# Performance work log

Measured on AMD Instinct MI355X. Metric: run time of the kernel, lower is better.

## Reference

```python
import jax, jax.numpy as jnp
import numpy as np

D = 1024
H = 16
F = 4096
EPS = 1e-6


def _layernorm(x, alpha, bias):
    # Faithful to torch: unbiased std (ddof=1), divide by (std + eps)
    mean = jnp.mean(x, axis=-1, keepdims=True)
    std = jnp.std(x, axis=-1, keepdims=True, ddof=1)
    return alpha * (x - mean) / (std + EPS) + bias


def setup_inputs() -> dict:
    key = jax.random.key(0)
    ks = jax.random.split(key, 12)
    B, S = 2, 2048
    s = 1.0 / np.sqrt(D)
    inp = {
        "x": jax.random.normal(ks[0], (B, S, D), jnp.float32),
        "mask": jnp.ones((B, 1, 1, S), jnp.int32),
        "wq": jax.random.normal(ks[1], (D, D), jnp.float32) * s,
        "bq": jnp.zeros((D,), jnp.float32),
        "wk": jax.random.normal(ks[2], (D, D), jnp.float32) * s,
        "bk": jnp.zeros((D,), jnp.float32),
        "wv": jax.random.normal(ks[3], (D, D), jnp.float32) * s,
        "bv": jnp.zeros((D,), jnp.float32),
        "wo": jax.random.normal(ks[4], (D, D), jnp.float32) * s,
        "bo": jnp.zeros((D,), jnp.float32),
        "ln1_a": jnp.ones((D,), jnp.float32),
        "ln1_b": jnp.zeros((D,), jnp.float32),
        "ln2_a": jnp.ones((D,), jnp.float32),
        "ln2_b": jnp.zeros((D,), jnp.float32),
        "w1": jax.random.normal(ks[5], (D, F), jnp.float32) * s,
        "b1": jnp.zeros((F,), jnp.float32),
        "w2": jax.random.normal(ks[6], (F, D), jnp.float32) * (1.0 / np.sqrt(F)),
        "b2": jnp.zeros((D,), jnp.float32),
    }
    return inp


def reference(x, mask, wq, bq, wk, bk, wv, bv, wo, bo,
              ln1_a, ln1_b, ln2_a, ln2_b, w1, b1, w2, b2):
    B, S, _ = x.shape
    dk = D // H
    # --- residual 1: pre-LN self-attention ---
    h = _layernorm(x, ln1_a, ln1_b)
    q = (h @ wq + bq).reshape(B, S, H, dk).transpose(0, 2, 1, 3)
    k = (h @ wk + bk).reshape(B, S, H, dk).transpose(0, 2, 1, 3)
    v = (h @ wv + bv).reshape(B, S, H, dk).transpose(0, 2, 1, 3)
    scores = jnp.einsum('bhqd,bhkd->bhqk', q, k) / jnp.sqrt(jnp.float32(dk))
    scores = jnp.where(mask == 0, jnp.float32(-1e9), scores)
    attn = jax.nn.softmax(scores, axis=-1)
    ctx = jnp.einsum('bhqk,bhkd->bhqd', attn, v)
    ctx = ctx.transpose(0, 2, 1, 3).reshape(B, S, D)
    x = x + (ctx @ wo + bo)
    # --- residual 2: pre-LN feed-forward ---
    h = _layernorm(x, ln2_a, ln2_b)
    ff = jax.nn.relu(h @ w1 + b1) @ w2 + b2
    return x + ff
```

## Files before the change

### kernel.cpp

```cpp
#include <hip/hip_runtime.h>
#include <hip/hip_bf16.h>
#include <math.h>

typedef __attribute__((ext_vector_type(8))) short bf16x8;
typedef __attribute__((ext_vector_type(4))) float f32x4;
typedef unsigned int uint32;
typedef __attribute__((ext_vector_type(2))) unsigned int uint32x2;

#define DMODEL 1024
#define SEQ    2048
#define NB     2
#define NH     16
#define HD     64
#define FDIM   4096
#define NTOK   (NB*SEQ)

__device__ __forceinline__ void async16(const void* g, void* s) {
    __builtin_amdgcn_global_load_lds((const __attribute__((address_space(1))) unsigned int*)g,
                                     (__attribute__((address_space(3))) unsigned int*)s,
                                     16, 0, 0);
}

__global__ __launch_bounds__(256) void transpose_cvt_k(const float* __restrict__ src,
                                                       __hip_bfloat16* __restrict__ dst,
                                                       int R, int C) {
    __shared__ __hip_bfloat16 tile[32][33];
    int tx = threadIdx.x, ty = threadIdx.y;
    int bx = blockIdx.x * 32, by = blockIdx.y * 32;
    for (int i = 0; i < 32; i += 8)
        tile[ty + i][tx] = __float2bfloat16(src[(size_t)(by + ty + i) * C + bx + tx]);
    __syncthreads();
    for (int i = 0; i < 32; i += 8)
        dst[(size_t)(bx + ty + i) * R + by + tx] = tile[tx][ty + i];
}

__global__ __launch_bounds__(256) void ln_kernel(const float* __restrict__ x,
                                                 const float* __restrict__ alpha,
                                                 const float* __restrict__ beta,
                                                 __hip_bfloat16* __restrict__ out) {
    const int row = blockIdx.x, tid = threadIdx.x;
    const size_t base = (size_t)row * DMODEL;
    float v[4];
    for (int e = 0; e < 4; ++e) v[e] = x[base + tid * 4 + e];
    float s1 = v[0] + v[1] + v[2] + v[3];
    float s2 = v[0]*v[0] + v[1]*v[1] + v[2]*v[2] + v[3]*v[3];
    for (int off = 32; off > 0; off >>= 1) {
        s1 += __shfl_down(s1, off);
        s2 += __shfl_down(s2, off);
    }
    __shared__ float red[8];
    int w = tid >> 6, lane = tid & 63;
    if (lane == 0) { red[w * 2] = s1; red[w * 2 + 1] = s2; }
    __syncthreads();
    if (tid == 0) {
        float a = 0.f, b = 0.f;
        for (int i = 0; i < 4; ++i) { a += red[2 * i]; b += red[2 * i + 1]; }
        red[0] = a; red[1] = b;
    }
    __syncthreads();
    s1 = red[0]; s2 = red[1];
    float mean = s1 * (1.0f / DMODEL);
    float var  = fmaxf((s2 - (float)DMODEL * mean * mean) * (1.0f / (DMODEL - 1)), 0.f);
    float inv  = 1.0f / (sqrtf(var) + 1e-6f);
    for (int e = 0; e < 4; ++e) {
        int c = tid * 4 + e;
        float y = alpha[c] * (v[e] - mean) * inv + beta[c];
        out[base + c] = __float2bfloat16(y);
    }
}

template <int EPI>
__global__ __launch_bounds__(256) void gemm_bt(const __hip_bfloat16* __restrict__ A,
                                               const __hip_bfloat16* __restrict__ Bt,
                                               const float* __restrict__ bias,
                                               const float* __restrict__ res,
                                               void* __restrict__ Cout,
                                               int M, int N, int K) {
    __shared__ alignas(16) __hip_bfloat16 As[2][128 * 32];
    __shared__ alignas(16) __hip_bfloat16 Bs[2][128 * 32];
    const int tid = threadIdx.x, l = tid & 63;
    const int w = tid >> 6;
    const int wm = w >> 1, wn = w & 1, quad = l >> 4, lc = l & 15;
    const int row0 = blockIdx.y * 128, col0 = blockIdx.x * 128;
    const int lr = l >> 2, cb = l & 3;
    const int srow = 32 * w + lr;
    const int scol = (cb ^ ((lr >> 1) & 3)) * 8;
    const int rsw  = (lc >> 1) & 3;

    f32x4 acc[4][4];
    for (int i = 0; i < 4; ++i)
        for (int j = 0; j < 4; ++j) acc[i][j] = (f32x4){0.f, 0.f, 0.f, 0.f};

    for (int c = 0; c < 2; ++c) {
        async16(A  + (size_t)(row0 + srow + 16 * c) * K + scol, (char*)&As[0][0] + w * 2048 + c * 1024);
        async16(Bt + (size_t)(col0 + srow + 16 * c) * K + scol, (char*)&Bs[0][0] + w * 2048 + c * 1024);
    }
    const int NKT = K / 32;
    for (int kt = 0; kt < NKT; ++kt) {
        const int cur = kt & 1;
        __syncthreads();
        if (kt + 1 < NKT) {
            const int k1 = (kt + 1) * 32;
            for (int c = 0; c < 2; ++c) {
                async16(A  + (size_t)(row0 + srow + 16 * c) * K + k1 + scol, (char*)&As[cur ^ 1][0] + w * 2048 + c * 1024);
                async16(Bt + (size_t)(col0 + srow + 16 * c) * K + k1 + scol, (char*)&Bs[cur ^ 1][0] + w * 2048 + c * 1024);
            }
        }
        bf16x8 af[4], bfr[4];
        for (int i = 0; i < 4; ++i) af[i]  = *(const bf16x8*)&As[cur][(64 * wm + 16 * i + lc) * 32 + (quad ^ rsw) * 8];
        for (int j = 0; j < 4; ++j) bfr[j] = *(const bf16x8*)&Bs[cur][(64 * wn + 16 * j + lc) * 32 + (quad ^ rsw) * 8];
        for (int i = 0; i < 4; ++i)
            for (int j = 0; j < 4; ++j)
                acc[i][j] = __builtin_amdgcn_mfma_f32_16x16x32_bf16(af[i], bfr[j], acc[i][j], 0, 0, 0);
    }

    __hip_bfloat16* Cb = (__hip_bfloat16*)Cout;
    float* Cf = (float*)Cout;
    for (int j = 0; j < 4; ++j) {
        int col = col0 + 64 * wn + 16 * j + lc;
        float bv = bias[col];
        for (int i = 0; i < 4; ++i) {
            int rbase = row0 + 64 * wm + 16 * i + quad * 4;
            for (int r = 0; r < 4; ++r) {
                size_t idx = (size_t)(rbase + r) * N + col;
                float vacc = acc[i][j][r] + bv;
                if (EPI == 0)      Cb[idx] = __float2bfloat16(vacc);
                else if (EPI == 1) Cb[idx] = __float2bfloat16(fmaxf(vacc, 0.f));
                else               Cf[idx] = vacc + res[idx];
            }
        }
    }
}

template <int EPI>
__global__ __launch_bounds__(512) void gemm_bt_sk(const __hip_bfloat16* __restrict__ A,
                                                  const __hip_bfloat16* __restrict__ Bt,
                                                  const float* __restrict__ bias,
                                                  const float* __restrict__ res,
                                                  void* __restrict__ Cout,
                                                  int M, int N, int K) {
    __shared__ alignas(16) char smem[65536];
    const int tid = threadIdx.x, l = tid & 63;
    const int w = tid >> 6;
    const int g = w >> 2;
    const int wl = w & 3;
    const int wm = wl >> 1, wn = wl & 1, quad = l >> 4, lc = l & 15;
    const int row0 = blockIdx.y * 128, col0 = blockIdx.x * 128;
    const int lr = l >> 2, cb = l & 3;
    const int srow = 32 * wl + lr;
    const int scol = (cb ^ ((lr >> 1) & 3)) * 8;
    const int rsw  = (lc >> 1) & 3;
    const int Kh = K >> 1;
    const int kbase = g * Kh;

    char* AsBase = smem + (size_t)g * 16384;
    char* BsBase = smem + 32768 + (size_t)g * 16384;

    f32x4 acc[4][4];
    for (int i = 0; i < 4; ++i)
        for (int j = 0; j < 4; ++j) acc[i][j] = (f32x4){0.f, 0.f, 0.f, 0.f};

    for (int c = 0; c < 2; ++c) {
        async16(A  + (size_t)(row0 + srow + 16 * c) * K + kbase + scol, AsBase + wl * 2048 + c * 1024);
        async16(Bt + (size_t)(col0 + srow + 16 * c) * K + kbase + scol, BsBase + wl * 2048 + c * 1024);
    }
    const int NKT = Kh / 32;
    for (int kt = 0; kt < NKT; ++kt) {
        const int cur = kt & 1;
        __syncthreads();
        if (kt + 1 < NKT) {
            const int k1 = kbase + (kt + 1) * 32;
            for (int c = 0; c < 2; ++c) {
                async16(A  + (size_t)(row0 + srow + 16 * c) * K + k1 + scol, AsBase + (cur ^ 1) * 8192 + wl * 2048 + c * 1024);
                async16(Bt + (size_t)(col0 + srow + 16 * c) * K + k1 + scol, BsBase + (cur ^ 1) * 8192 + wl * 2048 + c * 1024);
            }
        }
        const __hip_bfloat16* Asc = (const __hip_bfloat16*)(AsBase + cur * 8192);
        const __hip_bfloat16* Bsc = (const __hip_bfloat16*)(BsBase + cur * 8192);
        bf16x8 af[4], bfr[4];
        for (int i = 0; i < 4; ++i) af[i]  = *(const bf16x8*)&Asc[(64 * wm + 16 * i + lc) * 32 + (quad ^ rsw) * 8];
        for (int j = 0; j < 4; ++j) bfr[j] = *(const bf16x8*)&Bsc[(64 * wn + 16 * j + lc) * 32 + (quad ^ rsw) * 8];
        for (int i = 0; i < 4; ++i)
            for (int j = 0; j < 4; ++j)
                acc[i][j] = __builtin_amdgcn_mfma_f32_16x16x32_bf16(af[i], bfr[j], acc[i][j], 0, 0, 0);
    }

    __syncthreads();
    float* comb = (float*)smem;
    if (g == 1) {
        for (int j = 0; j < 4; ++j) {
            int col = 64 * wn + 16 * j + lc;
            int ccol = col ^ ((quad & 1) << 4);
            for (int i = 0; i < 4; ++i) {
                int rb = 64 * wm + 16 * i + quad * 4;
                for (int r = 0; r < 4; ++r)
                    comb[(rb + r) * 128 + ccol] = acc[i][j][r];
            }
        }
    }
    __syncthreads();
    if (g == 0) {
        __hip_bfloat16* Cb = (__hip_bfloat16*)Cout;
        float* Cf = (float*)Cout;
        for (int j = 0; j < 4; ++j) {
            int coll = 64 * wn + 16 * j + lc;
            int ccol = coll ^ ((quad & 1) << 4);
            int col  = col0 + coll;
            float bv = bias[col];
            for (int i = 0; i < 4; ++i) {
                int rbl = 64 * wm + 16 * i + quad * 4;
                for (int r = 0; r < 4; ++r) {
                    size_t idx = (size_t)(row0 + rbl + r) * N + col;
                    float vacc = acc[i][j][r] + comb[(rbl + r) * 128 + ccol] + bv;
                    if (EPI == 0)      Cb[idx] = __float2bfloat16(vacc);
                    else if (EPI == 1) Cb[idx] = __float2bfloat16(fmaxf(vacc, 0.f));
                    else               Cf[idx] = vacc + res[idx];
                }
            }
        }
    }
}

__global__ __launch_bounds__(256) void gemm_qkv(const __hip_bfloat16* __restrict__ A,
                                                const __hip_bfloat16* __restrict__ Bt,
                                                const float* __restrict__ bq,
                                                const float* __restrict__ bk,
                                                const float* __restrict__ bv,
                                                __hip_bfloat16* __restrict__ qout,
                                                __hip_bfloat16* __restrict__ kout,
                                                __hip_bfloat16* __restrict__ vTout) {
    const int K = DMODEL;
    __shared__ alignas(16) __hip_bfloat16 As[2][128 * 32];
    __shared__ alignas(16) __hip_bfloat16 Bs[2][128 * 32];
    const int tid = threadIdx.x, l = tid & 63;
    const int w = tid >> 6;
    const int wm = w >> 1, wn = w & 1, quad = l >> 4, lc = l & 15;
    const int row0 = blockIdx.y * 128, col0 = blockIdx.x * 128;
    const int lr = l >> 2, cb = l & 3;
    const int srow = 32 * w + lr;
    const int scol = (cb ^ ((lr >> 1) & 3)) * 8;
    const int rsw  = (lc >> 1) & 3;

    f32x4 acc[4][4];
    for (int i = 0; i < 4; ++i)
        for (int j = 0; j < 4; ++j) acc[i][j] = (f32x4){0.f, 0.f, 0.f, 0.f};

    for (int c = 0; c < 2; ++c) {
        async16(A  + (size_t)(row0 + srow + 16 * c) * K + scol, (char*)&As[0][0] + w * 2048 + c * 1024);
        async16(Bt + (size_t)(col0 + srow + 16 * c) * K + scol, (char*)&Bs[0][0] + w * 2048 + c * 1024);
    }
    const int NKT = K / 32;
    for (int kt = 0; kt < NKT; ++kt) {
        const int cur = kt & 1;
        __syncthreads();
        if (kt + 1 < NKT) {
            const int k1 = (kt + 1) * 32;
            for (int c = 0; c < 2; ++c) {
                async16(A  + (size_t)(row0 + srow + 16 * c) * K + k1 + scol, (char*)&As[cur ^ 1][0] + w * 2048 + c * 1024);
                async16(Bt + (size_t)(col0 + srow + 16 * c) * K + k1 + scol, (char*)&Bs[cur ^ 1][0] + w * 2048 + c * 1024);
            }
        }
        bf16x8 af[4], bfr[4];
        for (int i = 0; i < 4; ++i) af[i]  = *(const bf16x8*)&As[cur][(64 * wm + 16 * i + lc) * 32 + (quad ^ rsw) * 8];
        for (int j = 0; j < 4; ++j) bfr[j] = *(const bf16x8*)&Bs[cur][(64 * wn + 16 * j + lc) * 32 + (quad ^ rsw) * 8];
        for (int i = 0; i < 4; ++i)
            for (int j = 0; j < 4; ++j)
                acc[i][j] = __builtin_amdgcn_mfma_f32_16x16x32_bf16(af[i], bfr[j], acc[i][j], 0, 0, 0);
    }

    const int seg = col0 >> 10;
    const float* bias = (seg == 0) ? bq : (seg == 1) ? bk : bv;
    for (int j = 0; j < 4; ++j) {
        int col  = col0 + 64 * wn + 16 * j + lc;
        int colm = col & (DMODEL - 1);
        float bvx = bias[colm];
        for (int i = 0; i < 4; ++i) {
            int rbase = row0 + 64 * wm + 16 * i + quad * 4;
            for (int r = 0; r < 4; ++r) {
                int trow = rbase + r;
                float vacc = acc[i][j][r] + bvx;
                if (seg == 2) {
                    int bb = trow >> 11, s = trow & (SEQ - 1);
                    int hh = colm >> 6, d = colm & (HD - 1);
                    vTout[((size_t)(bb * NH + hh) * HD + d) * SEQ + s] = __float2bfloat16(vacc);
                } else {
                    __hip_bfloat16* dst = (seg == 0) ? qout : kout;
                    dst[(size_t)trow * DMODEL + colm] = __float2bfloat16(vacc);
                }
            }
        }
    }
}

__global__ __launch_bounds__(512) void attn_kernel(const __hip_bfloat16* __restrict__ q,
                                                   const __hip_bfloat16* __restrict__ k,
                                                   const __hip_bfloat16* __restrict__ vT,
                                                   const int* __restrict__ mask,
                                                   __hip_bfloat16* __restrict__ ctx) {
    const int qt = blockIdx.x, bh = blockIdx.y;
    const int b = bh >> 4;
    const int q0 = qt * 128;
    const int tid = threadIdx.x, w = tid >> 6, l = tid & 63, quad = l >> 4, lc = l & 15;
    const int g = w >> 2, wl = w & 3;

    __shared__ alignas(16) char smem[65536];
    __hip_bfloat16* KhB = (__hip_bfloat16*)(smem + (size_t)g * 32768);
    __hip_bfloat16* VhB = (__hip_bfloat16*)(smem + (size_t)g * 32768 + 16384);

    const size_t base   = (size_t)b * SEQ * DMODEL + (size_t)(bh & 15) * HD;
    const size_t vtbase = (size_t)bh * HD * SEQ;
    const int gk = g * (SEQ / 2);

    bf16x8 qf[2][2];
    for (int s = 0; s < 2; ++s) {
        const __hip_bfloat16* qrow = &q[base + (size_t)(q0 + s * 64 + wl * 16 + lc) * DMODEL];
        qf[s][0] = *(const bf16x8*)&qrow[quad * 8];
        qf[s][1] = *(const bf16x8*)&qrow[32 + quad * 8];
    }

    f32x4 o[2][4];
    for (int s = 0; s < 2; ++s)
        for (int dj = 0; dj < 4; ++dj) o[s][dj] = (f32x4){0.f, 0.f, 0.f, 0.f};
    float rsp2[2] = {0.f, 0.f};

    const int lr  = l >> 2, cb = l & 3;
    const int cbsw = ((cb ^ ((lr >> 1) & 3))) * 8;
    const int rsw  = (lc >> 1) & 3;

    for (int c = 0; c < 2; ++c) {
        const int W = wl * 2 + c;
        const int rr = (W & 3) * 16 + lr, cc8 = (W >> 2) * 32 + cbsw;
        async16(&k [base   + (size_t)(gk + rr) * DMODEL + cc8], (char*)KhB + W * 1024);
        async16(&vT[vtbase + (size_t)rr * SEQ + gk + cc8],      (char*)VhB + W * 1024);
    }

    const int NT = SEQ / 128;
    for (int kt = 0; kt < NT; ++kt) {
        const int k0 = gk + kt * 64;
        const int cur = kt & 1;

        __syncthreads();
        if (kt + 1 < NT) {
            const int k1 = k0 + 64;
            for (int c = 0; c < 2; ++c) {
                const int W = wl * 2 + c;
                const int rr = (W & 3) * 16 + lr, cc8 = (W >> 2) * 32 + cbsw;
                async16(&k [base   + (size_t)(k1 + rr) * DMODEL + cc8], (char*)KhB + (cur ^ 1) * 8192 + W * 1024);
                async16(&vT[vtbase + (size_t)rr * SEQ + k1 + cc8],      (char*)VhB + (cur ^ 1) * 8192 + W * 1024);
            }
        }
        float mb[4][4];
        for (int jn = 0; jn < 4; ++jn) {
            int4 mi = *(const int4*)&mask[b * SEQ + k0 + jn * 16 + quad * 4];
            mb[jn][0] = mi.x ? 0.f : -INFINITY;
            mb[jn][1] = mi.y ? 0.f : -INFINITY;
            mb[jn][2] = mi.z ? 0.f : -INFINITY;
            mb[jn][3] = mi.w ? 0.f : -INFINITY;
        }

        bf16x8 kf0[4], kf1[4];
        for (int jn = 0; jn < 4; ++jn) {
            kf0[jn] = *(const bf16x8*)&KhB[(cur * 2 + 0) * 2048 + (jn * 16 + lc) * 32 + (quad ^ rsw) * 8];
            kf1[jn] = *(const bf16x8*)&KhB[(cur * 2 + 1) * 2048 + (jn * 16 + lc) * 32 + (quad ^ rsw) * 8];
        }
        bf16x8 vf0[4], vf1[4];
        for (int dj = 0; dj < 4; ++dj) {
            vf0[dj] = *(const bf16x8*)&VhB[(cur * 2 + 0) * 2048 + (dj * 16 + lc) * 32 + (quad ^ rsw) * 8];
            vf1[dj] = *(const bf16x8*)&VhB[(cur * 2 + 1) * 2048 + (dj * 16 + lc) * 32 + (quad ^ rsw) * 8];
        }

        for (int s = 0; s < 2; ++s) {
            f32x4 sa[4];
            __builtin_amdgcn_s_setprio(1);
            for (int jn = 0; jn < 4; ++jn) {
                f32x4 z = (f32x4){0.f, 0.f, 0.f, 0.f};
                z = __builtin_amdgcn_mfma_f32_16x16x32_bf16(kf0[jn], qf[s][0], z, 0, 0, 0);
                z = __builtin_amdgcn_mfma_f32_16x16x32_bf16(kf1[jn], qf[s][1], z, 0, 0, 0);
                sa[jn] = z;
            }
            __builtin_amdgcn_s_setprio(0);

            uint32 wd[4][2];
            float accs = 0.f;
            for (int jn = 0; jn < 4; ++jn) {
                float p0 = __expf(fmaf(sa[jn][0], 0.125f, mb[jn][0]));
                float p1 = __expf(fmaf(sa[jn][1], 0.125f, mb[jn][1]));
                float p2 = __expf(fmaf(sa[jn][2], 0.125f, mb[jn][2]));
                float p3 = __expf(fmaf(sa[jn][3], 0.125f, mb[jn][3]));
                accs += (p0 + p1) + (p2 + p3);
                __hip_bfloat16 h0 = __float2bfloat16(p0), h1 = __float2bfloat16(p1);
                __hip_bfloat16 h2 = __float2bfloat16(p2), h3 = __float2bfloat16(p3);
                wd[jn][0] = (uint32)*(unsigned short*)&h0 | ((uint32)*(unsigned short*)&h1 << 16);
                wd[jn][1] = (uint32)*(unsigned short*)&h2 | ((uint32)*(unsigned short*)&h3 << 16);
            }
            rsp2[s] += accs;

            union { uint32 u[4]; bf16x8 v8; } pf0, pf1;
            for (int p = 0; p < 2; ++p) {
                uint32x2 a = __builtin_amdgcn_permlane32_swap(wd[0][p], wd[1][p], false, false);
                uint32x2 r = __builtin_amdgcn_permlane16_swap(a[0], a[1], false, false);
                pf0.u[p] = r[0]; pf0.u[2 + p] = r[1];
                uint32x2 a2 = __builtin_amdgcn_permlane32_swap(wd[2][p], wd[3][p], false, false);
                uint32x2 r2 = __builtin_amdgcn_permlane16_swap(a2[0], a2[1], false, false);
                pf1.u[p] = r2[0]; pf1.u[2 + p] = r2[1];
            }

            __builtin_amdgcn_s_setprio(1);
            for (int dj = 0; dj < 4; ++dj) {
                o[s][dj] = __builtin_amdgcn_mfma_f32_16x16x32_bf16(pf0.v8, vf0[dj], o[s][dj], 0, 0, 0);
                o[s][dj] = __builtin_amdgcn_mfma_f32_16x16x32_bf16(pf1.v8, vf1[dj], o[s][dj], 0, 0, 0);
            }
            __builtin_amdgcn_s_setprio(0);
        }
    }

    __syncthreads();
    float* combo = (float*)smem;
    float* crs   = (float*)(smem + 33792);
    if (g == 1) {
        for (int s = 0; s < 2; ++s) {
            crs[(wl * 64 + l) * 2 + s] = rsp2[s];
            for (int dj = 0; dj < 4; ++dj)
                for (int r = 0; r < 4; ++r)
                    combo[(s * 64 + wl * 16 + quad * 4 + r) * 66 + dj * 16 + lc] = o[s][dj][r];
        }
    }
    __syncthreads();
    if (g == 0) {
        for (int s = 0; s < 2; ++s) {
            float rs = rsp2[s] + crs[(wl * 64 + l) * 2 + s];
            rs += __shfl_xor(rs, 16);
            rs += __shfl_xor(rs, 32);
            for (int r = 0; r < 4; ++r) {
                float rq = __shfl(rs, (l & 48) | (quad * 4 + r));
                float linv = 1.0f / rq;
                int row = q0 + s * 64 + wl * 16 + quad * 4 + r;
                for (int dj = 0; dj < 4; ++dj) {
                    float ov = o[s][dj][r] + combo[(s * 64 + wl * 16 + quad * 4 + r) * 66 + dj * 16 + lc];
                    ctx[base + (size_t)row * DMODEL + dj * 16 + lc] = __float2bfloat16(ov * linv);
                }
            }
        }
    }
}

extern "C" void kernel_launch(void* const* d_in, const int* in_sizes, int n_in,
                              void* d_out, int out_size, void* d_ws, size_t ws_size,
                              hipStream_t stream) {
    const float* x    = (const float*)d_in[0];
    const int*   mask = (const int*)d_in[1];
    const float* wq = (const float*)d_in[2];
    const float* bq = (const float*)d_in[3];
    const float* wk = (const float*)d_in[4];
    const float* bk = (const float*)d_in[5];
    const float* wv = (const float*)d_in[6];
    const float* bv = (const float*)d_in[7];
    const float* wo = (const float*)d_in[8];
    const float* bo = (const float*)d_in[9];
    const float* ln1_a = (const float*)d_in[10];
    const float* ln1_b = (const float*)d_in[11];
    const float* ln2_a = (const float*)d_in[12];
    const float* ln2_b = (const float*)d_in[13];
    const float* w1 = (const float*)d_in[14];
    const float* b1 = (const float*)d_in[15];
    const float* w2 = (const float*)d_in[16];
    const float* b2 = (const float*)d_in[17];
    float* out = (float*)d_out;

    char* ws = (char*)d_ws;
    const size_t SZ_WT  = (size_t)DMODEL * DMODEL * 2;
    const size_t SZ_ACT = (size_t)NTOK * DMODEL * 2;
    const size_t SZ_WF  = (size_t)FDIM * DMODEL * 2;
    size_t off = 0;
    __hip_bfloat16* wqkvT = (__hip_bfloat16*)(ws + off); off += 3 * SZ_WT;
    __hip_bfloat16* woT   = (__hip_bfloat16*)(ws + off); off += SZ_WT;
    __hip_bfloat16* w1T   = (__hip_bfloat16*)(ws + off); off += SZ_WF;
    __hip_bfloat16* w2T   = (__hip_bfloat16*)(ws + off); off += SZ_WF;
    __hip_bfloat16* h1    = (__hip_bfloat16*)(ws + off); off += SZ_ACT;
    __hip_bfloat16* qb    = (__hip_bfloat16*)(ws + off); off += SZ_ACT;
    __hip_bfloat16* kb    = (__hip_bfloat16*)(ws + off); off += SZ_ACT;
    __hip_bfloat16* vTb   = (__hip_bfloat16*)(ws + off); off += SZ_ACT;
    __hip_bfloat16* ctx   = (__hip_bfloat16*)(ws + off); off += SZ_ACT;
    float*          x1    = (float*)(ws + off);          off += (size_t)NTOK * DMODEL * 4;
    __hip_bfloat16* h2    = (__hip_bfloat16*)(ws + off); off += SZ_ACT;
    __hip_bfloat16* ff1   = h1;

    dim3 tb(32, 8);
    transpose_cvt_k<<<dim3(32, 32), tb, 0, stream>>>(wq, wqkvT,                   DMODEL, DMODEL);
    transpose_cvt_k<<<dim3(32, 32), tb, 0, stream>>>(wk, wqkvT + 1024 * DMODEL,   DMODEL, DMODEL);
    transpose_cvt_k<<<dim3(32, 32), tb, 0, stream>>>(wv, wqkvT + 2048 * DMODEL,   DMODEL, DMODEL);
    transpose_cvt_k<<<dim3(32, 32), tb, 0, stream>>>(wo, woT, DMODEL, DMODEL);
    transpose_cvt_k<<<dim3(128, 32), tb, 0, stream>>>(w1, w1T, DMODEL, FDIM);
    transpose_cvt_k<<<dim3(32, 128), tb, 0, stream>>>(w2, w2T, FDIM, DMODEL);

    ln_kernel<<<NTOK, 256, 0, stream>>>(x, ln1_a, ln1_b, h1);

    gemm_qkv<<<dim3(3 * DMODEL / 128, NTOK / 128), 256, 0, stream>>>(h1, wqkvT, bq, bk, bv, qb, kb, vTb);

    attn_kernel<<<dim3(SEQ / 128, NB * NH), 512, 0, stream>>>(qb, kb, vTb, mask, ctx);

    gemm_bt_sk<2><<<dim3(DMODEL / 128, NTOK / 128), 512, 0, stream>>>(ctx, woT, bo, x, x1, NTOK, DMODEL, DMODEL);

    ln_kernel<<<NTOK, 256, 0, stream>>>(x1, ln2_a, ln2_b, h2);

    gemm_bt<1><<<dim3(FDIM / 128, NTOK / 128), 256, 0, stream>>>(h2, w1T, b1, nullptr, ff1, NTOK, FDIM, DMODEL);
    gemm_bt_sk<2><<<dim3(DMODEL / 128, NTOK / 128), 512, 0, stream>>>(ff1, w2T, b2, x1, out, NTOK, DMODEL, FDIM);
}
```

Before: 395.5 us.

## Double attention query tile per block, use exp2, fuse square weight transposes

Each attention block now handles 256 query rows instead of 128, so every K/V tile loaded into shared memory is reused across twice as many queries. The grid is reordered so consecutive blocks take different heads. The softmax exponent folds log2(e) into the scale and calls exp2f. The cross-group combine at the end runs in two passes so it fits the existing shared memory. The four square weight transposes are merged into one launch. Costs: more accumulator registers per thread (possible lower occupancy or spills) and half as many attention blocks in flight.

```diff
diff --git a/kernel.cpp b/kernel.cpp
--- a/kernel.cpp
+++ b/kernel.cpp
@@ -32,6 +32,25 @@
     __syncthreads();
     for (int i = 0; i < 32; i += 8)
         dst[(size_t)(bx + ty + i) * R + by + tx] = tile[tx][ty + i];
+}
+
+__global__ __launch_bounds__(256) void transpose_cvt4_k(const float* __restrict__ s0,
+                                                        const float* __restrict__ s1,
+                                                        const float* __restrict__ s2,
+                                                        const float* __restrict__ s3,
+                                                        __hip_bfloat16* __restrict__ d012,
+                                                        __hip_bfloat16* __restrict__ d3) {
+    __shared__ __hip_bfloat16 tile[32][33];
+    const int z = blockIdx.z;
+    const float* src = (z == 0) ? s0 : (z == 1) ? s1 : (z == 2) ? s2 : s3;
+    __hip_bfloat16* dst = (z < 3) ? d012 + (size_t)z * DMODEL * DMODEL : d3;
+    int tx = threadIdx.x, ty = threadIdx.y;
+    int bx = blockIdx.x * 32, by = blockIdx.y * 32;
+    for (int i = 0; i < 32; i += 8)
+        tile[ty + i][tx] = __float2bfloat16(src[(size_t)(by + ty + i) * DMODEL + bx + tx]);
+    __syncthreads();
+    for (int i = 0; i < 32; i += 8)
+        dst[(size_t)(bx + ty + i) * DMODEL + by + tx] = tile[tx][ty + i];
 }
 
 __global__ __launch_bounds__(256) void ln_kernel(const float* __restrict__ x,
@@ -297,9 +316,9 @@
                                                    const __hip_bfloat16* __restrict__ vT,
                                                    const int* __restrict__ mask,
                                                    __hip_bfloat16* __restrict__ ctx) {
-    const int qt = blockIdx.x, bh = blockIdx.y;
+    const int bh = blockIdx.x, qt = blockIdx.y;
     const int b = bh >> 4;
-    const int q0 = qt * 128;
+    const int q0 = qt * 256;
     const int tid = threadIdx.x, w = tid >> 6, l = tid & 63, quad = l >> 4, lc = l & 15;
     const int g = w >> 2, wl = w & 3;
 
@@ -311,21 +330,22 @@
     const size_t vtbase = (size_t)bh * HD * SEQ;
     const int gk = g * (SEQ / 2);
 
-    bf16x8 qf[2][2];
-    for (int s = 0; s < 2; ++s) {
+    bf16x8 qf[4][2];
+    for (int s = 0; s < 4; ++s) {
         const __hip_bfloat16* qrow = &q[base + (size_t)(q0 + s * 64 + wl * 16 + lc) * DMODEL];
         qf[s][0] = *(const bf16x8*)&qrow[quad * 8];
         qf[s][1] = *(const bf16x8*)&qrow[32 + quad * 8];
     }
 
-    f32x4 o[2][4];
-    for (int s = 0; s < 2; ++s)
+    f32x4 o[4][4];
+    for (int s = 0; s < 4; ++s)
         for (int dj = 0; dj < 4; ++dj) o[s][dj] = (f32x4){0.f, 0.f, 0.f, 0.f};
-    float rsp2[2] = {0.f, 0.f};
+    float rsp4[4] = {0.f, 0.f, 0.f, 0.f};
 
     const int lr  = l >> 2, cb = l & 3;
     const int cbsw = ((cb ^ ((lr >> 1) & 3))) * 8;
     const int rsw  = (lc >> 1) & 3;
+    const float SCL = 0.125f * 1.44269504f;
 
     for (int c = 0; c < 2; ++c) {
         const int W = wl * 2 + c;
@@ -369,7 +389,7 @@
             vf1[dj] = *(const bf16x8*)&VhB[(cur * 2 + 1) * 2048 + (dj * 16 + lc) * 32 + (quad ^ rsw) * 8];
         }
 
-        for (int s = 0; s < 2; ++s) {
+        for (int s = 0; s < 4; ++s) {
             f32x4 sa[4];
             __builtin_amdgcn_s_setprio(1);
             for (int jn = 0; jn < 4; ++jn) {
@@ -383,17 +403,17 @@
             uint32 wd[4][2];
             float accs = 0.f;
             for (int jn = 0; jn < 4; ++jn) {
-                float p0 = __expf(fmaf(sa[jn][0], 0.125f, mb[jn][0]));
-                float p1 = __expf(fmaf(sa[jn][1], 0.125f, mb[jn][1]));
-                float p2 = __expf(fmaf(sa[jn][2], 0.125f, mb[jn][2]));
-                float p3 = __expf(fmaf(sa[jn][3], 0.125f, mb[jn][3]));
+                float p0 = exp2f(fmaf(sa[jn][0], SCL, mb[jn][0]));
+                float p1 = exp2f(fmaf(sa[jn][1], SCL, mb[jn][1]));
+                float p2 = exp2f(fmaf(sa[jn][2], SCL, mb[jn][2]));
+                float p3 = exp2f(fmaf(sa[jn][3], SCL, mb[jn][3]));
                 accs += (p0 + p1) + (p2 + p3);
                 __hip_bfloat16 h0 = __float2bfloat16(p0), h1 = __float2bfloat16(p1);
                 __hip_bfloat16 h2 = __float2bfloat16(p2), h3 = __float2bfloat16(p3);
                 wd[jn][0] = (uint32)*(unsigned short*)&h0 | ((uint32)*(unsigned short*)&h1 << 16);
                 wd[jn][1] = (uint32)*(unsigned short*)&h2 | ((uint32)*(unsigned short*)&h3 << 16);
             }
-            rsp2[s] += accs;
+            rsp4[s] += accs;
 
             union { uint32 u[4]; bf16x8 v8; } pf0, pf1;
             for (int p = 0; p < 2; ++p) {
@@ -417,30 +437,35 @@
     __syncthreads();
     float* combo = (float*)smem;
     float* crs   = (float*)(smem + 33792);
-    if (g == 1) {
-        for (int s = 0; s < 2; ++s) {
-            crs[(wl * 64 + l) * 2 + s] = rsp2[s];
-            for (int dj = 0; dj < 4; ++dj)
-                for (int r = 0; r < 4; ++r)
-                    combo[(s * 64 + wl * 16 + quad * 4 + r) * 66 + dj * 16 + lc] = o[s][dj][r];
-        }
-    }
-    __syncthreads();
-    if (g == 0) {
-        for (int s = 0; s < 2; ++s) {
-            float rs = rsp2[s] + crs[(wl * 64 + l) * 2 + s];
-            rs += __shfl_xor(rs, 16);
-            rs += __shfl_xor(rs, 32);
-            for (int r = 0; r < 4; ++r) {
-                float rq = __shfl(rs, (l & 48) | (quad * 4 + r));
-                float linv = 1.0f / rq;
-                int row = q0 + s * 64 + wl * 16 + quad * 4 + r;
-                for (int dj = 0; dj < 4; ++dj) {
-                    float ov = o[s][dj][r] + combo[(s * 64 + wl * 16 + quad * 4 + r) * 66 + dj * 16 + lc];
-                    ctx[base + (size_t)row * DMODEL + dj * 16 + lc] = __float2bfloat16(ov * linv);
+    for (int pass = 0; pass < 2; ++pass) {
+        if (g == 1) {
+            for (int sh = 0; sh < 2; ++sh) {
+                int s = pass * 2 + sh;
+                crs[(wl * 64 + l) * 2 + sh] = rsp4[s];
+                for (int dj = 0; dj < 4; ++dj)
+                    for (int r = 0; r < 4; ++r)
+                        combo[(sh * 64 + wl * 16 + quad * 4 + r) * 66 + dj * 16 + lc] = o[s][dj][r];
+            }
+        }
+        __syncthreads();
+        if (g == 0) {
+            for (int sh = 0; sh < 2; ++sh) {
+                int s = pass * 2 + sh;
+                float rs = rsp4[s] + crs[(wl * 64 + l) * 2 + sh];
+                rs += __shfl_xor(rs, 16);
+                rs += __shfl_xor(rs, 32);
+                for (int r = 0; r < 4; ++r) {
+                    float rq = __shfl(rs, (l & 48) | (quad * 4 + r));
+                    float linv = 1.0f / rq;
+                    int row = q0 + s * 64 + wl * 16 + quad * 4 + r;
+                    for (int dj = 0; dj < 4; ++dj) {
+                        float ov = o[s][dj][r] + combo[(sh * 64 + wl * 16 + quad * 4 + r) * 66 + dj * 16 + lc];
+                        ctx[base + (size_t)row * DMODEL + dj * 16 + lc] = __float2bfloat16(ov * linv);
+                    }
                 }
             }
         }
+        __syncthreads();
     }
 }
 
@@ -486,10 +511,7 @@
     __hip_bfloat16* ff1   = h1;
 
     dim3 tb(32, 8);
-    transpose_cvt_k<<<dim3(32, 32), tb, 0, stream>>>(wq, wqkvT,                   DMODEL, DMODEL);
-    transpose_cvt_k<<<dim3(32, 32), tb, 0, stream>>>(wk, wqkvT + 1024 * DMODEL,   DMODEL, DMODEL);
-    transpose_cvt_k<<<dim3(32, 32), tb, 0, stream>>>(wv, wqkvT + 2048 * DMODEL,   DMODEL, DMODEL);
-    transpose_cvt_k<<<dim3(32, 32), tb, 0, stream>>>(wo, woT, DMODEL, DMODEL);
+    transpose_cvt4_k<<<dim3(32, 32, 4), tb, 0, stream>>>(wq, wk, wv, wo, wqkvT, woT);
     transpose_cvt_k<<<dim3(128, 32), tb, 0, stream>>>(w1, w1T, DMODEL, FDIM);
     transpose_cvt_k<<<dim3(32, 128), tb, 0, stream>>>(w2, w2T, FDIM, DMODEL);
 
@@ -497,7 +519,7 @@
 
     gemm_qkv<<<dim3(3 * DMODEL / 128, NTOK / 128), 256, 0, stream>>>(h1, wqkvT, bq, bk, bv, qb, kb, vTb);
 
-    attn_kernel<<<dim3(SEQ / 128, NB * NH), 512, 0, stream>>>(qb, kb, vTb, mask, ctx);
+    attn_kernel<<<dim3(NB * NH, SEQ / 256), 512, 0, stream>>>(qb, kb, vTb, mask, ctx);
 
     gemm_bt_sk<2><<<dim3(DMODEL / 128, NTOK / 128), 512, 0, stream>>>(ctx, woT, bo, x, x1, NTOK, DMODEL, DMODEL);
 
```

Result: no change. 393.2 us (-0.6%).
